# Kernel optimization log

Measured on AMD Instinct MI355X. Metric: run time of the kernel, lower is better.

Reference implementation:

```python
import jax, jax.numpy as jnp
import numpy as np

N = 50000
E = 800000
FEAT = 128
HID = 128
HEADS = 8
HEAD_DIM = HID // HEADS  # 16
NEG_SLOPE = 0.2


def _gat_layer(x, W, a_src, a_dst, b, src, dst, num_nodes):
    # x: [N, Fin]; W: [Fin, H*C]; a_src/a_dst: [H, C]; b: [H*C]
    H, C = a_src.shape
    h = (x @ W).reshape(num_nodes, H, C)               # [N,H,C]
    alpha_s = jnp.einsum('nhc,hc->nh', h, a_src)       # [N,H]
    alpha_d = jnp.einsum('nhc,hc->nh', h, a_dst)       # [N,H]
    e = jax.nn.leaky_relu(alpha_s[src] + alpha_d[dst], NEG_SLOPE)  # [E,H]
    # segment softmax over destination nodes (every node has a self-loop)
    m = jax.ops.segment_max(e, dst, num_segments=num_nodes)
    e = jnp.exp(e - m[dst])
    s = jax.ops.segment_sum(e, dst, num_segments=num_nodes)
    alpha = e / (s[dst] + 1e-16)                       # [E,H]
    msg = alpha[:, :, None] * h[src]                   # [E,H,C]
    out = jax.ops.segment_sum(msg, dst, num_segments=num_nodes)
    return out.reshape(num_nodes, H * C) + b


def setup_inputs() -> dict:
    key = jax.random.key(0)
    ks = jax.random.split(key, 12)
    x = jax.random.normal(ks[0], (N, FEAT), dtype=jnp.float32)
    edge_index = jax.random.randint(ks[1], (2, E), 0, N, dtype=jnp.int32)
    glorot = lambda k, shape: jax.random.uniform(
        k, shape, jnp.float32,
        -jnp.sqrt(6.0 / (shape[-2] + shape[-1])),
        jnp.sqrt(6.0 / (shape[-2] + shape[-1])))
    W1 = glorot(ks[2], (FEAT, HID))
    a_src1 = glorot(ks[3], (HEADS, HEAD_DIM))
    a_dst1 = glorot(ks[4], (HEADS, HEAD_DIM))
    b1 = jnp.zeros((HID,), jnp.float32)
    W2 = glorot(ks[5], (HID, HID))
    a_src2 = glorot(ks[6], (HEADS, HEAD_DIM))
    a_dst2 = glorot(ks[7], (HEADS, HEAD_DIM))
    b2 = jnp.zeros((HID,), jnp.float32)
    return {"x": x, "edge_index": edge_index,
            "W1": W1, "a_src1": a_src1, "a_dst1": a_dst1, "b1": b1,
            "W2": W2, "a_src2": a_src2, "a_dst2": a_dst2, "b2": b2}


def reference(x, edge_index, W1, a_src1, a_dst1, b1, W2, a_src2, a_dst2, b2):
    # GATConv adds self-loops to the (dense_to_sparse-derived) edge list
    loops = jnp.arange(N, dtype=edge_index.dtype)
    src = jnp.concatenate([edge_index[0], loops])
    dst = jnp.concatenate([edge_index[1], loops])
    h = _gat_layer(x, W1, a_src1, a_dst1, b1, src, dst, N)
    h = jax.nn.elu(h)
    # dropout: inference mode (training=False) -> identity
    h = _gat_layer(h, W2, a_src2, a_dst2, b2, src, dst, N)
    return jax.nn.elu(h)
```

## Files before the change

kernel.cpp:

```cpp
#include <hip/hip_runtime.h>
#include <hip/hip_fp16.h>
#include <math.h>

#define DEGMAX 64
#define CHUNK  2048
#define CAPB   6144

__global__ __launch_bounds__(256) void k_bin(
        const int* __restrict__ src, const int* __restrict__ dst, int E, int K,
        int* __restrict__ gcur, unsigned* __restrict__ bstore) {
    __shared__ int lcnt[256];
    __shared__ int gbase[256];
    int t = threadIdx.x;
    if (t < K) lcnt[t] = 0;
    __syncthreads();
    int e0 = blockIdx.x * CHUNK;
    unsigned pk[8]; short bk[8], rk[8];
    #pragma unroll
    for (int j = 0; j < 8; j++) {
        int e = e0 + t + j * 256;
        bool v = e < E;
        int s = v ? src[e] : 0;
        int d = v ? dst[e] : 0;
        int b = d >> 8;
        pk[j] = ((unsigned)(d & 255) << 16) | (unsigned)s;
        bk[j] = (short)b;
        rk[j] = v ? (short)atomicAdd(&lcnt[b], 1) : (short)-1;
    }
    __syncthreads();
    if (t < K) gbase[t] = lcnt[t] ? atomicAdd(&gcur[t], lcnt[t]) : 0;
    __syncthreads();
    #pragma unroll
    for (int j = 0; j < 8; j++) {
        if (rk[j] >= 0) {
            int b = bk[j];
            int pos = gbase[b] + rk[j];
            if (pos < CAPB) bstore[(size_t)b * CAPB + pos] = pk[j];
        }
    }
}

__global__ __launch_bounds__(256) void k_csr(
        const int* __restrict__ gcur, const unsigned* __restrict__ bstore,
        int N, int* __restrict__ cnt, int* __restrict__ offs,
        unsigned short* __restrict__ adj) {
    int b = blockIdx.x;
    int t = threadIdx.x;
    int n0 = b << 8;
    int nb = N - n0; if (nb > 256) nb = 256;
    int ecnt = gcur[b]; if (ecnt > CAPB) ecnt = CAPB;
    __shared__ int lcnt[256], lofs[256], wsum[4];
    __shared__ unsigned short stage[CAPB];
    const unsigned* bp = bstore + (size_t)b * CAPB;

    lcnt[t] = 0;
    __syncthreads();
    for (int i = t; i < ecnt; i += 256)
        atomicAdd(&lcnt[bp[i] >> 16], 1);
    __syncthreads();
    int mycnt = lcnt[t];
    int lane = t & 63, wv = t >> 6;
    int x = mycnt;
    #pragma unroll
    for (int d = 1; d < 64; d <<= 1) {
        int y = __shfl_up(x, d);
        if (lane >= d) x += y;
    }
    if (lane == 63) wsum[wv] = x;
    __syncthreads();
    int base = 0;
    for (int k = 0; k < wv; k++) base += wsum[k];
    int myofs = base + x - mycnt;
    lofs[t] = myofs;
    if (t < nb) {
        cnt[n0 + t]  = mycnt;
        offs[n0 + t] = b * CAPB + myofs;
    }
    __syncthreads();
    lcnt[t] = 0;
    __syncthreads();
    for (int i = t; i < ecnt; i += 256) {
        unsigned p = bp[i];
        int node = p >> 16;
        int r = atomicAdd(&lcnt[node], 1);
        stage[lofs[node] + r] = (unsigned short)(p & 0xffffu);
    }
    __syncthreads();
    for (int i = t; i < ecnt; i += 256)
        adj[(size_t)b * CAPB + i] = stage[i];
}

__device__ inline float4 ld4f(const float* p) { return *(const float4*)p; }
__device__ inline float4 ld4f(const __half* p) {
    uint2 u = *(const uint2*)p;
    float2 f0 = __half22float2(*(__half2*)&u.x);
    float2 f1 = __half22float2(*(__half2*)&u.y);
    return make_float4(f0.x, f0.y, f1.x, f1.y);
}

template<typename InT>
__global__ __launch_bounds__(256) void k_gemm_fused(
        const InT* __restrict__ X, const float* __restrict__ W,
        const float* __restrict__ a_src, const float* __restrict__ a_dst,
        __half* __restrict__ H16, float* __restrict__ as_out,
        float* __restrict__ ad_out, int M) {
    __shared__ float xs[64][17];
    __shared__ float ws[16][128];
    int t = threadIdx.x;
    int row0 = blockIdx.x * 64;
    float acc[8][4];
    #pragma unroll
    for (int i = 0; i < 8; i++)
        #pragma unroll
        for (int j = 0; j < 4; j++) acc[i][j] = 0.f;
    int rg = (t >> 5) * 8;
    int cg = (t & 31) * 4;

    for (int k0 = 0; k0 < 128; k0 += 16) {
        {
            int r = t >> 2;
            int kk = (t & 3) * 4;
            int gr = row0 + r;
            float4 v = make_float4(0.f, 0.f, 0.f, 0.f);
            if (gr < M) v = ld4f(&X[(size_t)gr * 128 + k0 + kk]);
            xs[r][kk + 0] = v.x; xs[r][kk + 1] = v.y;
            xs[r][kk + 2] = v.z; xs[r][kk + 3] = v.w;
        }
        {
            #pragma unroll
            for (int p = 0; p < 2; p++) {
                int kk = (t >> 5) + p * 8;
                int cc = (t & 31) * 4;
                *(float4*)&ws[kk][cc] = *(const float4*)&W[(size_t)(k0 + kk) * 128 + cc];
            }
        }
        __syncthreads();
        #pragma unroll
        for (int k = 0; k < 16; k++) {
            float4 wv = *(const float4*)&ws[k][cg];
            #pragma unroll
            for (int i = 0; i < 8; i++) {
                float xv = xs[rg + i][k];
                acc[i][0] += xv * wv.x; acc[i][1] += xv * wv.y;
                acc[i][2] += xv * wv.z; acc[i][3] += xv * wv.w;
            }
        }
        __syncthreads();
    }

    float4 As4 = *(const float4*)&a_src[cg];
    float4 Ad4 = *(const float4*)&a_dst[cg];
    int h = (t & 31) >> 2;
    #pragma unroll
    for (int i = 0; i < 8; i++) {
        int gr = row0 + rg + i;
        if (gr < M) {
            __half2 p0 = __floats2half2_rn(acc[i][0], acc[i][1]);
            __half2 p1 = __floats2half2_rn(acc[i][2], acc[i][3]);
            unsigned u0 = *(unsigned*)&p0, u1 = *(unsigned*)&p1;
            *(uint2*)&H16[(size_t)gr * 128 + cg] = make_uint2(u0, u1);
        }
        float ps = acc[i][0]*As4.x + acc[i][1]*As4.y + acc[i][2]*As4.z + acc[i][3]*As4.w;
        float pd = acc[i][0]*Ad4.x + acc[i][1]*Ad4.y + acc[i][2]*Ad4.z + acc[i][3]*Ad4.w;
        ps += __shfl_xor(ps, 1); ps += __shfl_xor(ps, 2);
        pd += __shfl_xor(pd, 1); pd += __shfl_xor(pd, 2);
        if ((t & 3) == 0 && gr < M) {
            as_out[gr * 8 + h] = ps;
            ad_out[gr * 8 + h] = pd;
        }
    }
}

template<typename OutT>
__global__ __launch_bounds__(256) void k_aggregate(
        const __half* __restrict__ H, const float* __restrict__ as_,
        const float* __restrict__ ad_, const int* __restrict__ cnt,
        const int* __restrict__ offs, const unsigned short* __restrict__ adj,
        const float* __restrict__ bias, OutT* __restrict__ out, int N) {
    int wave = (int)((blockIdx.x * blockDim.x + threadIdx.x) >> 6);
    int lane = threadIdx.x & 63;
    if (wave >= N) return;
    int n = wave;
    int hd = lane >> 3;
    int deg = cnt[n]; if (deg > DEGMAX) deg = DEGMAX;
    int row = offs[n];
    int sv = (lane < deg) ? (int)adj[row + lane] : n;
    float adv = ad_[n * 8 + (lane & 7)];

    float vs = as_[n * 8 + hd] + ad_[n * 8 + hd];
    vs = vs > 0.f ? vs : 0.2f * vs;
    float wsf = __expf(vs);
    unsigned hrs = *(const unsigned*)&H[(size_t)n * 128 + lane * 2];
    float2 hvs = __half22float2(*(__half2*)&hrs);
    float ssum = wsf, ax = wsf * hvs.x, ay = wsf * hvs.y;

    for (int i = 0; i < deg; i += 8) {
        int e = i + (lane >> 3);
        bool val = e < deg;
        int se = __shfl(sv, val ? e : 0);
        float lgt = as_[(size_t)se * 8 + (lane & 7)];
        float v = lgt + adv;
        v = v > 0.f ? v : 0.2f * v;
        float w = val ? __expf(v) : 0.f;
        int sj[8]; unsigned hraw[8];
        #pragma unroll
        for (int j = 0; j < 8; j++) {
            int idx = i + j; if (idx >= deg) idx = deg - 1;
            sj[j] = __shfl(sv, idx);
        }
        #pragma unroll
        for (int j = 0; j < 8; j++)
            hraw[j] = *(const unsigned*)&H[(size_t)sj[j] * 128 + lane * 2];
        #pragma unroll
        for (int j = 0; j < 8; j++) {
            float wj = __shfl(w, j * 8 + hd);
            float2 hv = __half22float2(*(__half2*)&hraw[j]);
            ssum += wj; ax += wj * hv.x; ay += wj * hv.y;
        }
    }
    float inv = 1.f / (ssum + 1e-16f);
    float ox = ax * inv + bias[lane * 2];
    float oy = ay * inv + bias[lane * 2 + 1];
    ox = ox > 0.f ? ox : __expf(ox) - 1.f;
    oy = oy > 0.f ? oy : __expf(oy) - 1.f;
    if constexpr (sizeof(OutT) == 2) {
        __half2 hv = __floats2half2_rn(ox, oy);
        *(__half2*)&out[(size_t)n * 128 + lane * 2] = hv;
    } else {
        *(float2*)&out[(size_t)n * 128 + lane * 2] = make_float2(ox, oy);
    }
}

static inline char* bump(char*& w, size_t bytes) {
    char* p = w;
    w += (bytes + 255) & ~(size_t)255;
    return p;
}

extern "C" void kernel_launch(void* const* d_in, const int* in_sizes, int n_in,
                              void* d_out, int out_size, void* d_ws, size_t ws_size,
                              hipStream_t stream) {
    const float* x   = (const float*)d_in[0];
    const int*   ei  = (const int*)d_in[1];
    const float* W1  = (const float*)d_in[2];
    const float* as1 = (const float*)d_in[3];
    const float* ad1 = (const float*)d_in[4];
    const float* b1  = (const float*)d_in[5];
    const float* W2  = (const float*)d_in[6];
    const float* as2 = (const float*)d_in[7];
    const float* ad2 = (const float*)d_in[8];
    const float* b2  = (const float*)d_in[9];
    float* out = (float*)d_out;

    int N = in_sizes[0] / 128;
    int E = in_sizes[1] / 2;
    const int* srcs = ei;
    const int* dsts = ei + E;
    int K = (N + 255) >> 8;

    char* w = (char*)d_ws;
    int*            cnt   = (int*)           bump(w, (size_t)N * sizeof(int));
    int*            offs  = (int*)           bump(w, (size_t)N * sizeof(int));
    int*            gcur  = (int*)           bump(w, 256 * sizeof(int));
    unsigned*       bst   = (unsigned*)      bump(w, (size_t)256 * CAPB * sizeof(unsigned));
    unsigned short* adj   = (unsigned short*)bump(w, (size_t)256 * CAPB * sizeof(unsigned short));
    __half*         H16   = (__half*)        bump(w, (size_t)N * 128 * sizeof(__half));
    __half*         A16   = (__half*)        bump(w, (size_t)N * 128 * sizeof(__half));
    float*          asb   = (float*)         bump(w, (size_t)N * 8 * sizeof(float));
    float*          adb   = (float*)         bump(w, (size_t)N * 8 * sizeof(float));

    hipMemsetAsync(gcur, 0, 256 * sizeof(int), stream);
    k_bin<<<(E + CHUNK - 1) / CHUNK, 256, 0, stream>>>(srcs, dsts, E, K, gcur, bst);
    k_csr<<<K, 256, 0, stream>>>(gcur, bst, N, cnt, offs, adj);

    k_gemm_fused<float><<<(N + 63) / 64, 256, 0, stream>>>(x, W1, as1, ad1, H16, asb, adb, N);
    k_aggregate<__half><<<(N + 3) / 4, 256, 0, stream>>>(H16, asb, adb, cnt, offs, adj, b1, A16, N);

    k_gemm_fused<__half><<<(N + 63) / 64, 256, 0, stream>>>(A16, W2, as2, ad2, H16, asb, adb, N);
    k_aggregate<float><<<(N + 3) / 4, 256, 0, stream>>>(H16, asb, adb, cnt, offs, adj, b2, out, N);
}
```

Measured before the change: 262.4 us.

## Use fp16 MFMA for the dense projection and prefetch neighbor rows in aggregation

```diff
diff --git a/kernel.cpp b/kernel.cpp
--- a/kernel.cpp
+++ b/kernel.cpp
@@ -5,6 +5,9 @@
 #define DEGMAX 64
 #define CHUNK  2048
 #define CAPB   6144
+
+typedef _Float16 half8 __attribute__((ext_vector_type(8)));
+typedef float    f32x4 __attribute__((ext_vector_type(4)));
 
 __global__ __launch_bounds__(256) void k_bin(
         const int* __restrict__ src, const int* __restrict__ dst, int E, int K,
@@ -90,86 +93,118 @@
         adj[(size_t)b * CAPB + i] = stage[i];
 }
 
+__global__ void k_wcast(const float* __restrict__ W, __half* __restrict__ Wfrag) {
+    int id = blockIdx.x * blockDim.x + threadIdx.x;
+    if (id >= 2048) return;
+    int lane = id & 63;
+    int ct = (id >> 6) & 7;
+    int kc = id >> 9;
+    int q = lane >> 4, n = lane & 15;
+    #pragma unroll
+    for (int j = 0; j < 8; j++) {
+        int k = kc * 32 + q * 8 + j;
+        int c = ct * 16 + n;
+        Wfrag[(size_t)id * 8 + j] = __float2half(W[(size_t)k * 128 + c]);
+    }
+}
+
 __device__ inline float4 ld4f(const float* p) { return *(const float4*)p; }
-__device__ inline float4 ld4f(const __half* p) {
-    uint2 u = *(const uint2*)p;
-    float2 f0 = __half22float2(*(__half2*)&u.x);
-    float2 f1 = __half22float2(*(__half2*)&u.y);
-    return make_float4(f0.x, f0.y, f1.x, f1.y);
-}
 
 template<typename InT>
-__global__ __launch_bounds__(256) void k_gemm_fused(
-        const InT* __restrict__ X, const float* __restrict__ W,
+__global__ __launch_bounds__(256) void k_gemm_mfma(
+        const InT* __restrict__ X, const __half* __restrict__ Wfrag,
         const float* __restrict__ a_src, const float* __restrict__ a_dst,
         __half* __restrict__ H16, float* __restrict__ as_out,
         float* __restrict__ ad_out, int M) {
-    __shared__ float xs[64][17];
-    __shared__ float ws[16][128];
+    __shared__ __half xls[64][136];
     int t = threadIdx.x;
+    int w = t >> 6, lane = t & 63;
+    int q = lane >> 4, n = lane & 15;
     int row0 = blockIdx.x * 64;
-    float acc[8][4];
-    #pragma unroll
-    for (int i = 0; i < 8; i++)
-        #pragma unroll
-        for (int j = 0; j < 4; j++) acc[i][j] = 0.f;
-    int rg = (t >> 5) * 8;
-    int cg = (t & 31) * 4;
-
-    for (int k0 = 0; k0 < 128; k0 += 16) {
-        {
-            int r = t >> 2;
-            int kk = (t & 3) * 4;
-            int gr = row0 + r;
-            float4 v = make_float4(0.f, 0.f, 0.f, 0.f);
-            if (gr < M) v = ld4f(&X[(size_t)gr * 128 + k0 + kk]);
-            xs[r][kk + 0] = v.x; xs[r][kk + 1] = v.y;
-            xs[r][kk + 2] = v.z; xs[r][kk + 3] = v.w;
-        }
-        {
+
+    half8 bfrag[4][2];
+    #pragma unroll
+    for (int kc = 0; kc < 4; kc++)
+        #pragma unroll
+        for (int c2 = 0; c2 < 2; c2++) {
+            int ct = w * 2 + c2;
+            uint4 u = *(const uint4*)(Wfrag + (((size_t)(kc * 8 + ct)) * 64 + lane) * 8);
+            bfrag[kc][c2] = *(half8*)&u;
+        }
+
+    #pragma unroll
+    for (int rep = 0; rep < 8; rep++) {
+        int lin = rep * 1024 + t * 4;
+        int r = lin >> 7, k = lin & 127;
+        int gr = row0 + r;
+        uint2 u;
+        if constexpr (sizeof(InT) == 4) {
+            float4 v = (gr < M) ? ld4f((const float*)&X[(size_t)gr * 128 + k])
+                                : make_float4(0.f, 0.f, 0.f, 0.f);
+            __half2 h0 = __floats2half2_rn(v.x, v.y);
+            __half2 h1 = __floats2half2_rn(v.z, v.w);
+            u = make_uint2(*(unsigned*)&h0, *(unsigned*)&h1);
+        } else {
+            u = (gr < M) ? *(const uint2*)&X[(size_t)gr * 128 + k] : make_uint2(0, 0);
+        }
+        *(uint2*)&xls[r][k] = u;
+    }
+    __syncthreads();
+
+    f32x4 acc[4][2];
+    #pragma unroll
+    for (int rt = 0; rt < 4; rt++)
+        #pragma unroll
+        for (int c2 = 0; c2 < 2; c2++)
+            acc[rt][c2] = (f32x4){0.f, 0.f, 0.f, 0.f};
+
+    #pragma unroll
+    for (int kc = 0; kc < 4; kc++)
+        #pragma unroll
+        for (int rt = 0; rt < 4; rt++) {
+            uint4 au = *(const uint4*)&xls[rt * 16 + n][kc * 32 + q * 8];
+            half8 af = *(half8*)&au;
+            acc[rt][0] = __builtin_amdgcn_mfma_f32_16x16x32_f16(af, bfrag[kc][0], acc[rt][0], 0, 0, 0);
+            acc[rt][1] = __builtin_amdgcn_mfma_f32_16x16x32_f16(af, bfrag[kc][1], acc[rt][1], 0, 0, 0);
+        }
+
+    #pragma unroll
+    for (int c2 = 0; c2 < 2; c2++) {
+        int h = w * 2 + c2;
+        float avs = a_src[h * 16 + n];
+        float avd = a_dst[h * 16 + n];
+        #pragma unroll
+        for (int rt = 0; rt < 4; rt++)
             #pragma unroll
-            for (int p = 0; p < 2; p++) {
-                int kk = (t >> 5) + p * 8;
-                int cc = (t & 31) * 4;
-                *(float4*)&ws[kk][cc] = *(const float4*)&W[(size_t)(k0 + kk) * 128 + cc];
+            for (int reg = 0; reg < 4; reg++) {
+                int grow = row0 + rt * 16 + q * 4 + reg;
+                float val = acc[rt][c2][reg];
+                if (grow < M) H16[(size_t)grow * 128 + h * 16 + n] = __float2half(val);
+                float ps = val * avs, pd = val * avd;
+                ps += __shfl_xor(ps, 1); ps += __shfl_xor(ps, 2);
+                ps += __shfl_xor(ps, 4); ps += __shfl_xor(ps, 8);
+                pd += __shfl_xor(pd, 1); pd += __shfl_xor(pd, 2);
+                pd += __shfl_xor(pd, 4); pd += __shfl_xor(pd, 8);
+                if (n == 0 && grow < M) {
+                    as_out[grow * 8 + h] = ps;
+                    ad_out[grow * 8 + h] = pd;
+                }
             }
-        }
-        __syncthreads();
-        #pragma unroll
-        for (int k = 0; k < 16; k++) {
-            float4 wv = *(const float4*)&ws[k][cg];
-            #pragma unroll
-            for (int i = 0; i < 8; i++) {
-                float xv = xs[rg + i][k];
-                acc[i][0] += xv * wv.x; acc[i][1] += xv * wv.y;
-                acc[i][2] += xv * wv.z; acc[i][3] += xv * wv.w;
-            }
-        }
-        __syncthreads();
-    }
-
-    float4 As4 = *(const float4*)&a_src[cg];
-    float4 Ad4 = *(const float4*)&a_dst[cg];
-    int h = (t & 31) >> 2;
-    #pragma unroll
-    for (int i = 0; i < 8; i++) {
-        int gr = row0 + rg + i;
-        if (gr < M) {
-            __half2 p0 = __floats2half2_rn(acc[i][0], acc[i][1]);
-            __half2 p1 = __floats2half2_rn(acc[i][2], acc[i][3]);
-            unsigned u0 = *(unsigned*)&p0, u1 = *(unsigned*)&p1;
-            *(uint2*)&H16[(size_t)gr * 128 + cg] = make_uint2(u0, u1);
-        }
-        float ps = acc[i][0]*As4.x + acc[i][1]*As4.y + acc[i][2]*As4.z + acc[i][3]*As4.w;
-        float pd = acc[i][0]*Ad4.x + acc[i][1]*Ad4.y + acc[i][2]*Ad4.z + acc[i][3]*Ad4.w;
-        ps += __shfl_xor(ps, 1); ps += __shfl_xor(ps, 2);
-        pd += __shfl_xor(pd, 1); pd += __shfl_xor(pd, 2);
-        if ((t & 3) == 0 && gr < M) {
-            as_out[gr * 8 + h] = ps;
-            ad_out[gr * 8 + h] = pd;
-        }
-    }
-}
+    }
+}
+
+#define LOADB(ii, LG, HR)                                                     \
+    {                                                                         \
+        int e_ = (ii) + (lane >> 3);                                          \
+        int se_ = __shfl(sv, (e_ < deg) ? e_ : 0);                            \
+        LG = as_[(size_t)se_ * 8 + (lane & 7)];                               \
+        _Pragma("unroll")                                                     \
+        for (int j_ = 0; j_ < 8; j_++) {                                      \
+            int idx_ = (ii) + j_; if (idx_ >= deg) idx_ = deg - 1;            \
+            int sj_ = __shfl(sv, idx_);                                       \
+            HR[j_] = *(const unsigned*)&H[(size_t)sj_ * 128 + lane * 2];      \
+        }                                                                     \
+    }
 
 template<typename OutT>
 __global__ __launch_bounds__(256) void k_aggregate(
@@ -194,29 +229,24 @@
     float2 hvs = __half22float2(*(__half2*)&hrs);
     float ssum = wsf, ax = wsf * hvs.x, ay = wsf * hvs.y;
 
+    float lgt_c; unsigned hraw_c[8];
+    if (deg > 0) LOADB(0, lgt_c, hraw_c);
     for (int i = 0; i < deg; i += 8) {
-        int e = i + (lane >> 3);
-        bool val = e < deg;
-        int se = __shfl(sv, val ? e : 0);
-        float lgt = as_[(size_t)se * 8 + (lane & 7)];
-        float v = lgt + adv;
+        float lgt_n; unsigned hraw_n[8];
+        int inext = i + 8;
+        if (inext < deg) LOADB(inext, lgt_n, hraw_n);
+        float v = lgt_c + adv;
         v = v > 0.f ? v : 0.2f * v;
-        float w = val ? __expf(v) : 0.f;
-        int sj[8]; unsigned hraw[8];
+        float wgt = (i + (lane >> 3) < deg) ? __expf(v) : 0.f;
         #pragma unroll
         for (int j = 0; j < 8; j++) {
-            int idx = i + j; if (idx >= deg) idx = deg - 1;
-            sj[j] = __shfl(sv, idx);
-        }
-        #pragma unroll
-        for (int j = 0; j < 8; j++)
-            hraw[j] = *(const unsigned*)&H[(size_t)sj[j] * 128 + lane * 2];
-        #pragma unroll
-        for (int j = 0; j < 8; j++) {
-            float wj = __shfl(w, j * 8 + hd);
-            float2 hv = __half22float2(*(__half2*)&hraw[j]);
+            float wj = __shfl(wgt, j * 8 + hd);
+            float2 hv = __half22float2(*(__half2*)&hraw_c[j]);
             ssum += wj; ax += wj * hv.x; ay += wj * hv.y;
         }
+        lgt_c = lgt_n;
+        #pragma unroll
+        for (int j = 0; j < 8; j++) hraw_c[j] = hraw_n[j];
     }
     float inv = 1.f / (ssum + 1e-16f);
     float ox = ax * inv + bias[lane * 2];
@@ -268,14 +298,18 @@
     __half*         A16   = (__half*)        bump(w, (size_t)N * 128 * sizeof(__half));
     float*          asb   = (float*)         bump(w, (size_t)N * 8 * sizeof(float));
     float*          adb   = (float*)         bump(w, (size_t)N * 8 * sizeof(float));
+    __half*         Wf1   = (__half*)        bump(w, 16384 * sizeof(__half));
+    __half*         Wf2   = (__half*)        bump(w, 16384 * sizeof(__half));
 
     hipMemsetAsync(gcur, 0, 256 * sizeof(int), stream);
+    k_wcast<<<8, 256, 0, stream>>>(W1, Wf1);
+    k_wcast<<<8, 256, 0, stream>>>(W2, Wf2);
     k_bin<<<(E + CHUNK - 1) / CHUNK, 256, 0, stream>>>(srcs, dsts, E, K, gcur, bst);
     k_csr<<<K, 256, 0, stream>>>(gcur, bst, N, cnt, offs, adj);
 
-    k_gemm_fused<float><<<(N + 63) / 64, 256, 0, stream>>>(x, W1, as1, ad1, H16, asb, adb, N);
+    k_gemm_mfma<float><<<(N + 63) / 64, 256, 0, stream>>>(x, Wf1, as1, ad1, H16, asb, adb, N);
     k_aggregate<__half><<<(N + 3) / 4, 256, 0, stream>>>(H16, asb, adb, cnt, offs, adj, b1, A16, N);
 
-    k_gemm_fused<__half><<<(N + 63) / 64, 256, 0, stream>>>(A16, W2, as2, ad2, H16, asb, adb, N);
+    k_gemm_mfma<__half><<<(N + 63) / 64, 256, 0, stream>>>(A16, Wf2, as2, ad2, H16, asb, adb, N);
     k_aggregate<float><<<(N + 3) / 4, 256, 0, stream>>>(H16, asb, adb, cnt, offs, adj, b2, out, N);
 }
```

New measurement: 234.4 us. 10.7% less time.
